# Performance work log

Hardware: AMD Instinct MI355X
Metric: run time of the kernel (lower is better)

The kernel has to match this reference:

```python
import jax, jax.numpy as jnp
import numpy as np

N = 10000
E = 160000
F_IN = 2000
HEADS = 10
C1 = 128      # layer-1 per-head out channels
C2 = 128      # layer-2 per-head out channels (latent_dim)
NEG_SLOPE = 0.2
EPS = 1e-16


def gat_conv(x, W, att_src, att_dst, bias, src, dst, heads, out_ch, concat):
    """PyG-style GATConv (eval mode, self-loops already included in src/dst).
    x: [N, F_in]; W: [F_in, heads*out_ch]; att_*: [heads, out_ch]; bias: [out_dim].
    src/dst: [E'] edge endpoints (message flows src -> dst).
    """
    n = x.shape[0]
    h = (x @ W).reshape(n, heads, out_ch)              # [N, H, C]
    a_src = jnp.einsum('nhc,hc->nh', h, att_src)       # [N, H]
    a_dst = jnp.einsum('nhc,hc->nh', h, att_dst)       # [N, H]
    e = a_src[src] + a_dst[dst]                        # [E', H]
    e = jax.nn.leaky_relu(e, NEG_SLOPE)
    # segment softmax over incoming edges of each destination node
    m = jax.ops.segment_max(e, dst, num_segments=n)    # [N, H]
    ex = jnp.exp(e - m[dst])
    s = jax.ops.segment_sum(ex, dst, num_segments=n)   # [N, H]
    alpha = ex / (s[dst] + EPS)                        # [E', H]
    msg = h[src] * alpha[:, :, None]                   # [E', H, C]
    out = jax.ops.segment_sum(msg, dst, num_segments=n)  # [N, H, C]
    out = out.reshape(n, heads * out_ch) if concat else out.mean(axis=1)
    return out + bias


def setup_inputs() -> dict:
    key = jax.random.key(0)
    ks = jax.random.split(key, 10)
    glorot = lambda k, shape: jax.random.normal(k, shape, jnp.float32) * np.sqrt(2.0 / (shape[0] + shape[-1]))
    x = jax.random.normal(ks[0], (N, F_IN), jnp.float32)
    edge_index = jax.random.randint(ks[1], (2, E), 0, N, jnp.int64)
    W1 = glorot(ks[2], (F_IN, HEADS * C1))
    att_src1 = glorot(ks[3], (HEADS, C1))
    att_dst1 = glorot(ks[4], (HEADS, C1))
    b1 = jnp.zeros((HEADS * C1,), jnp.float32)
    W2 = glorot(ks[5], (HEADS * C1, HEADS * C2))
    att_src2 = glorot(ks[6], (HEADS, C2))
    att_dst2 = glorot(ks[7], (HEADS, C2))
    b2 = jnp.zeros((C2,), jnp.float32)
    return dict(x=x, edge_index=edge_index, W1=W1, att_src1=att_src1,
                att_dst1=att_dst1, b1=b1, W2=W2, att_src2=att_src2,
                att_dst2=att_dst2, b2=b2)


def reference(x, edge_index, W1, att_src1, att_dst1, b1, W2, att_src2, att_dst2, b2):
    n = x.shape[0]
    loops = jnp.arange(n, dtype=edge_index.dtype)
    src = jnp.concatenate([edge_index[0], loops])  # add self-loops (PyG default)
    dst = jnp.concatenate([edge_index[1], loops])
    h = jax.nn.relu(gat_conv(x, W1, att_src1, att_dst1, b1, src, dst, HEADS, C1, True))
    z = jax.nn.relu(gat_conv(h, W2, att_src2, att_dst2, b2, src, dst, HEADS, C2, False))
    return z
```

## Files before the change

kernel.cpp:

```cpp
#include <hip/hip_runtime.h>

typedef unsigned short u16;
typedef __attribute__((ext_vector_type(8))) short bf16x8;
typedef __attribute__((ext_vector_type(4))) float f32x4;
typedef __attribute__((ext_vector_type(4))) unsigned u32x4;

#define NN    10000
#define EE    160000
#define ET    170000
#define FIN   2000
#define MPAD  10112
#define K1PAD 2048
#define NH    1280
#define HEADS 10
#define NT    10
#define NWG   790

__device__ __forceinline__ u16 f32_to_bf16(float f) {
    unsigned u = __float_as_uint(f);
    unsigned r = (u + 0x7fffu + ((u >> 16) & 1u)) >> 16;
    return (u16)r;
}
__device__ __forceinline__ float bf16lo(unsigned pv) { return __uint_as_float(pv << 16); }
__device__ __forceinline__ float bf16hi(unsigned pv) { return __uint_as_float(pv & 0xffff0000u); }

__device__ __forceinline__ void gload16(const u16* g, u16* l) {
    __builtin_amdgcn_global_load_lds(
        (const __attribute__((address_space(1))) void*)g,
        (__attribute__((address_space(3))) void*)l, 16, 0, 0);
}


__global__ __launch_bounds__(256) void k_conv_x(const float* __restrict__ x,
                                                uint2* __restrict__ A1) {
    const int total = MPAD * (K1PAD / 4);
    for (int idx = blockIdx.x * 256 + threadIdx.x; idx < total; idx += gridDim.x * 256) {
        int r = idx >> 9;
        int c = (idx & 511) << 2;
        float4 v = make_float4(0.f, 0.f, 0.f, 0.f);
        if (r < NN && c < FIN) v = *(const float4*)(x + (size_t)r * FIN + c);
        uint2 p;
        p.x = (unsigned)f32_to_bf16(v.x) | ((unsigned)f32_to_bf16(v.y) << 16);
        p.y = (unsigned)f32_to_bf16(v.z) | ((unsigned)f32_to_bf16(v.w) << 16);
        A1[idx] = p;
    }
}

__global__ __launch_bounds__(256) void k_convT(const float* __restrict__ W,
                                               u16* __restrict__ Bt,
                                               int K, int Nn, int Kpad) {
    __shared__ float tile[32][33];
    int k0 = blockIdx.x * 32, n0 = blockIdx.y * 32;
    int tx = threadIdx.x, ty = threadIdx.y;
    #pragma unroll
    for (int i = 0; i < 32; i += 8) {
        int k = k0 + ty + i;
        tile[ty + i][tx] = (k < K) ? W[(size_t)k * Nn + n0 + tx] : 0.f;
    }
    __syncthreads();
    #pragma unroll
    for (int i = 0; i < 32; i += 8) {
        int n = n0 + ty + i, k = k0 + tx;
        Bt[(size_t)n * Kpad + k] = f32_to_bf16(tile[tx][ty + i]);
    }
}


template <bool AHM>
__global__ __launch_bounds__(512) void k_gemm(const u16* __restrict__ A,
                                              const u16* __restrict__ Bt,
                                              u16* __restrict__ Chm,
                                              const int Kpad, const int kTiles) {
    __shared__ __attribute__((aligned(16))) u16 S[32768];
    const int bid = blockIdx.x;
    const int xcd = bid & 7, idx = bid >> 3;
    const int q = NWG >> 3, r = NWG & 7;
    const int L = (xcd < r) ? (xcd * (q + 1) + idx)
                            : (r * (q + 1) + (xcd - r) * q + idx);
    const size_t m0 = (size_t)(L / NT) * 128, n0 = (size_t)(L % NT) * 128;

    const int t = threadIdx.x;
    const int lane = t & 63;
    const int wave = t >> 6;
    const int wr = wave >> 2, wc = wave & 3;

    f32x4 acc[4][2] = {};

    const int srow = t >> 3;
    const int klocal = (((t & 7) ^ ((t >> 3) & 7)) << 3);
    const u16* aRow = AHM ? (A + (m0 + srow) * 128 + klocal)
                          : (A + (m0 + srow) * (size_t)Kpad + klocal);
    const u16* bRow = Bt + (n0 + srow) * (size_t)Kpad + klocal;
    const size_t aStep = AHM ? (size_t)64 * 128 : (size_t)64 * Kpad;
    const size_t bStep = (size_t)64 * Kpad;

#define STAGE(kt_, bufb_) do {                                                   \
        char* db = (char*)S + (bufb_) + wave * 1024;                             \
        const u16* aP;                                                           \
        if (AHM) aP = aRow + (size_t)((kt_) >> 1) * (MPAD << 7) + ((kt_) & 1) * 64; \
        else     aP = aRow + (size_t)(kt_) * 64;                                 \
        const u16* bP = bRow + (size_t)(kt_) * 64;                               \
        gload16(aP,         (u16*)(db));                                         \
        gload16(aP + aStep, (u16*)(db + 8192));                                  \
        gload16(bP,         (u16*)(db + 16384));                                 \
        gload16(bP + bStep, (u16*)(db + 24576));                                 \
    } while (0)

    STAGE(0, 0);

    const int rl = lane & 15;
    const int kchunk = lane >> 4;
    const int xorv = (rl & 7) << 4;
    const int aBase0 = (wr * 64 + rl) * 128;
    const int bBase0 = (wc * 32 + rl) * 128;
    const char* Sb = (const char*)S;

    for (int kt = 0; kt < kTiles; ++kt) {
        asm volatile("s_waitcnt vmcnt(0)" ::: "memory");
        __builtin_amdgcn_s_barrier();
        if (kt + 1 < kTiles) STAGE(kt + 1, ((kt + 1) & 1) * 32768);
        const int bufo = (kt & 1) * 32768;
        #pragma unroll
        for (int ks = 0; ks < 2; ++ks) {
            const int px = (ks * 64 + kchunk * 16) ^ xorv;
            bf16x8 af[4], bfr[2];
            #pragma unroll
            for (int mf = 0; mf < 4; ++mf)
                af[mf] = *(const bf16x8*)(Sb + bufo + aBase0 + mf * 2048 + px);
            #pragma unroll
            for (int nf = 0; nf < 2; ++nf)
                bfr[nf] = *(const bf16x8*)(Sb + bufo + 16384 + bBase0 + nf * 2048 + px);
            #pragma unroll
            for (int mf = 0; mf < 4; ++mf)
                #pragma unroll
                for (int nf = 0; nf < 2; ++nf)
                    acc[mf][nf] = __builtin_amdgcn_mfma_f32_16x16x32_bf16(
                        af[mf], bfr[nf], acc[mf][nf], 0, 0, 0);
        }
    }
#undef STAGE

    u16* Cb = Chm + (size_t)(n0 >> 7) * (MPAD << 7);
    #pragma unroll
    for (int mf = 0; mf < 4; ++mf)
        #pragma unroll
        for (int i = 0; i < 4; ++i) {
            size_t row = m0 + wr * 64 + mf * 16 + (lane >> 4) * 4 + i;
            u16* crow = Cb + row * 128 + wc * 32 + rl;
            #pragma unroll
            for (int nf = 0; nf < 2; ++nf)
                crow[nf * 16] = f32_to_bf16(acc[mf][nf][i]);
        }
}

__global__ __launch_bounds__(256) void k_attn(const u16* __restrict__ Hhm,
                                              const float* __restrict__ att_s,
                                              const float* __restrict__ att_d,
                                              float* __restrict__ a_src,
                                              float* __restrict__ a_dst) {
    const int lane = threadIdx.x & 63;
    const int n = blockIdx.x * 4 + (threadIdx.x >> 6);
    if (n >= NN) return;
    const unsigned* Hd = (const unsigned*)Hhm;
    #pragma unroll
    for (int h = 0; h < HEADS; ++h) {
        unsigned pv = Hd[((size_t)h * MPAD + n) * 64 + lane];
        float v0 = bf16lo(pv), v1 = bf16hi(pv);
        int c = h * 128 + lane * 2;
        float s = v0 * att_s[c] + v1 * att_s[c + 1];
        float d = v0 * att_d[c] + v1 * att_d[c + 1];
        #pragma unroll
        for (int o = 32; o; o >>= 1) { s += __shfl_xor(s, o); d += __shfl_xor(d, o); }
        if (lane == 0) { a_src[n * HEADS + h] = s; a_dst[n * HEADS + h] = d; }
    }
}

__global__ void k_count(const int* __restrict__ ei, int* __restrict__ deg) {
    int e = blockIdx.x * blockDim.x + threadIdx.x;
    if (e >= ET) return;
    int d = (e < EE) ? ei[EE + e] : (e - EE);
    atomicAdd(&deg[d], 1);
}

__global__ __launch_bounds__(256) void k_scan(const int* __restrict__ deg,
                                              int* __restrict__ off,
                                              int* __restrict__ cursor) {
    __shared__ int wt[4];
    const int t = threadIdx.x, lane = t & 63, w = t >> 6;
    const int lo = t * 40;
    const int hi = (lo + 40 < NN) ? lo + 40 : NN;
    int s = 0;
    for (int i = lo; i < hi; ++i) s += deg[i];
    int x = s;
    #pragma unroll
    for (int o = 1; o < 64; o <<= 1) { int y = __shfl_up(x, o); if (lane >= o) x += y; }
    if (lane == 63) wt[w] = x;
    __syncthreads();
    int wp = 0;
    for (int k = 0; k < w; ++k) wp += wt[k];
    int run = wp + x - s;
    for (int i = lo; i < hi; ++i) { off[i] = run; cursor[i] = run; run += deg[i]; }
    if (t == 255) off[NN] = wp + x;
}

__global__ void k_scatter(const int* __restrict__ ei, int* __restrict__ cursor,
                          int* __restrict__ csr_src, int* __restrict__ csr_dst) {
    int e = blockIdx.x * blockDim.x + threadIdx.x;
    if (e >= ET) return;
    int s = (e < EE) ? ei[e] : (e - EE);
    int d = (e < EE) ? ei[EE + e] : (e - EE);
    int pos = atomicAdd(&cursor[d], 1);
    csr_src[pos] = s;
    csr_dst[pos] = d;
}

__global__ __launch_bounds__(256) void k_edgew(const float* __restrict__ a_src,
                                               const float* __restrict__ a_dst,
                                               const int* __restrict__ csr_s,
                                               const int* __restrict__ csr_d,
                                               float* __restrict__ wbuf) {
    int i = blockIdx.x * 256 + threadIdx.x;
    if (i >= ET) return;
    const int s = csr_s[i], d = csr_d[i];
    const float* ps = a_src + (size_t)s * HEADS;
    const float* pd = a_dst + (size_t)d * HEADS;
    #pragma unroll
    for (int h = 0; h < HEADS; ++h) {
        float e = ps[h] + pd[h];
        e = (e >= 0.f) ? e : 0.2f * e;
        wbuf[(size_t)h * ET + i] = __expf(e);
    }
}

template <int LAYER>
__global__ __launch_bounds__(256) void k_agg(const u16* __restrict__ Hhm,
                                             const float* __restrict__ wbuf,
                                             const int* __restrict__ off,
                                             const int* __restrict__ csr,
                                             const float* __restrict__ bias,
                                             unsigned* __restrict__ outp) {
    const int bid = blockIdx.x;
    const int xcd = bid & 7, slot = bid >> 3;
    const int wv = threadIdx.x >> 6, lane = threadIdx.x & 63;
    const int u = slot * 4 + wv;
    if (u >= 3125) return;
    int h, qd;
    if (u < 2500) { h = xcd; qd = u; }
    else {
        int qg = xcd * 625 + (u - 2500);
        h = 8 + (qg >= 2500);
        qd = (qg >= 2500) ? qg - 2500 : qg;
    }
    const int g = lane >> 4, l = lane & 15;
    const int n = qd * 4 + g;
    const int beg = off[n], end = off[n + 1];
    const u16* Hh = Hhm + (size_t)h * (MPAD * 128);
    const float* wp = wbuf + (size_t)h * ET;

    float acc[8] = {};
    float den = 0.f;
    int i = beg;
    for (; i + 1 < end; i += 2) {
        const int s0 = csr[i], s1 = csr[i + 1];
        const float w0 = wp[i], w1 = wp[i + 1];
        const u32x4 v0 = *(const u32x4*)(Hh + (size_t)s0 * 128 + l * 8);
        const u32x4 v1 = *(const u32x4*)(Hh + (size_t)s1 * 128 + l * 8);
        den += w0 + w1;
        #pragma unroll
        for (int j = 0; j < 4; ++j) {
            acc[2 * j]     = fmaf(bf16lo(v0[j]), w0, acc[2 * j]);
            acc[2 * j + 1] = fmaf(bf16hi(v0[j]), w0, acc[2 * j + 1]);
            acc[2 * j]     = fmaf(bf16lo(v1[j]), w1, acc[2 * j]);
            acc[2 * j + 1] = fmaf(bf16hi(v1[j]), w1, acc[2 * j + 1]);
        }
    }
    if (i < end) {
        const int s0 = csr[i];
        const float w0 = wp[i];
        const u32x4 v0 = *(const u32x4*)(Hh + (size_t)s0 * 128 + l * 8);
        den += w0;
        #pragma unroll
        for (int j = 0; j < 4; ++j) {
            acc[2 * j]     = fmaf(bf16lo(v0[j]), w0, acc[2 * j]);
            acc[2 * j + 1] = fmaf(bf16hi(v0[j]), w0, acc[2 * j + 1]);
        }
    }
    const float si = 1.f / (den + 1e-16f);

    u32x4 pk;
    if (LAYER == 1) {
        const int c = h * 128 + l * 8;
        #pragma unroll
        for (int j = 0; j < 4; ++j) {
            float v0 = fmaxf(fmaf(acc[2 * j],     si, bias[c + 2 * j]),     0.f);
            float v1 = fmaxf(fmaf(acc[2 * j + 1], si, bias[c + 2 * j + 1]), 0.f);
            pk[j] = (unsigned)f32_to_bf16(v0) | ((unsigned)f32_to_bf16(v1) << 16);
        }
    } else {
        #pragma unroll
        for (int j = 0; j < 4; ++j) {
            pk[j] = (unsigned)f32_to_bf16(acc[2 * j] * si)
                  | ((unsigned)f32_to_bf16(acc[2 * j + 1] * si) << 16);
        }
    }
    *(u32x4*)(outp + (size_t)h * (MPAD * 64) + (size_t)n * 64 + l * 4) = pk;
}

__global__ __launch_bounds__(256) void k_zpad(unsigned* __restrict__ A2) {
    int idx = blockIdx.x * 256 + threadIdx.x;
    if (idx >= 10 * 112 * 64) return;
    int h = idx / 7168, r = idx - h * 7168;
    int row = NN + (r >> 6), dw = r & 63;
    A2[((size_t)h * MPAD + row) * 64 + dw] = 0u;
}

__global__ __launch_bounds__(256) void k_final(const unsigned* __restrict__ Z,
                                               const float* __restrict__ b2,
                                               float* __restrict__ out) {
    int t = blockIdx.x * 256 + threadIdx.x;
    if (t >= NN * 64) return;
    int n = t >> 6, d = t & 63;
    float s0 = 0.f, s1 = 0.f;
    #pragma unroll
    for (int h = 0; h < HEADS; ++h) {
        unsigned pv = Z[(size_t)h * (MPAD * 64) + (size_t)n * 64 + d];
        s0 += bf16lo(pv);
        s1 += bf16hi(pv);
    }
    float2 z;
    z.x = fmaxf(fmaf(s0, 0.1f, b2[2 * d]),     0.f);
    z.y = fmaxf(fmaf(s1, 0.1f, b2[2 * d + 1]), 0.f);
    *(float2*)(out + (size_t)n * 128 + 2 * d) = z;
}

extern "C" void kernel_launch(void* const* d_in, const int* in_sizes, int n_in,
                              void* d_out, int out_size, void* d_ws, size_t ws_size,
                              hipStream_t stream) {
    const float* x   = (const float*)d_in[0];
    const int*   ei  = (const int*)  d_in[1];
    const float* W1  = (const float*)d_in[2];
    const float* as1 = (const float*)d_in[3];
    const float* ad1 = (const float*)d_in[4];
    const float* b1  = (const float*)d_in[5];
    const float* W2  = (const float*)d_in[6];
    const float* as2 = (const float*)d_in[7];
    const float* ad2 = (const float*)d_in[8];
    const float* b2  = (const float*)d_in[9];

    char* ws = (char*)d_ws;
    const size_t A1_OFF  = 0;
    const size_t A2_OFF  = 0;
    const size_t B2T_OFF = (size_t)MPAD * NH * 2;
    const size_t WB_OFF  = B2T_OFF + (size_t)NH * NH * 2;
    const size_t H_OFF   = (size_t)MPAD * K1PAD * 2;
    const size_t B1T_OFF = H_OFF + (size_t)MPAD * NH * 2;
    size_t o = B1T_OFF + (size_t)NH * K1PAD * 2;
    const size_t AS_OFF  = o; o += 400128;
    const size_t AD_OFF  = o; o += 400128;
    const size_t DEG_OFF = o; o += 40064;
    const size_t OFF_OFF = o; o += 40064;
    const size_t CUR_OFF = o; o += 40064;
    const size_t CSR_OFF = o; o += 680064;
    const size_t CSD_OFF = o; o += 680064;
    if (ws_size < o) return;

    u16*      A1   = (u16*)(ws + A1_OFF);
    unsigned* A2   = (unsigned*)(ws + A2_OFF);
    u16*      B2t  = (u16*)(ws + B2T_OFF);
    float*    wbuf = (float*)(ws + WB_OFF);
    u16*      H    = (u16*)(ws + H_OFF);
    u16*      B1t  = (u16*)(ws + B1T_OFF);
    float*    aS   = (float*)(ws + AS_OFF);
    float*    aD   = (float*)(ws + AD_OFF);
    int*      deg  = (int*)(ws + DEG_OFF);
    int*      offp = (int*)(ws + OFF_OFF);
    int*      cur  = (int*)(ws + CUR_OFF);
    int*      csr  = (int*)(ws + CSR_OFF);
    int*      csd  = (int*)(ws + CSD_OFF);

    hipMemsetAsync(deg, 0, NN * sizeof(int), stream);
    k_count<<<(ET + 255) / 256, 256, 0, stream>>>(ei, deg);
    k_scan<<<1, 256, 0, stream>>>(deg, offp, cur);
    k_scatter<<<(ET + 255) / 256, 256, 0, stream>>>(ei, cur, csr, csd);

    k_conv_x<<<2048, 256, 0, stream>>>(x, (uint2*)A1);
    k_convT<<<dim3(K1PAD / 32, NH / 32), dim3(32, 8), 0, stream>>>(W1, B1t, FIN, NH, K1PAD);
    k_gemm<false><<<NWG, 512, 0, stream>>>(A1, B1t, H, K1PAD, K1PAD / 64);
    k_attn<<<2500, 256, 0, stream>>>(H, as1, ad1, aS, aD);
    k_edgew<<<(ET + 255) / 256, 256, 0, stream>>>(aS, aD, csr, csd, wbuf);
    k_agg<1><<<6256, 256, 0, stream>>>(H, wbuf, offp, csr, b1, A2);
    k_zpad<<<280, 256, 0, stream>>>(A2);

    k_convT<<<dim3(NH / 32, NH / 32), dim3(32, 8), 0, stream>>>(W2, B2t, NH, NH, NH);
    k_gemm<true><<<NWG, 512, 0, stream>>>((u16*)A2, B2t, H, NH, NH / 64);
    k_attn<<<2500, 256, 0, stream>>>(H, as2, ad2, aS, aD);
    k_edgew<<<(ET + 255) / 256, 256, 0, stream>>>(aS, aD, csr, csd, wbuf);
    k_agg<2><<<6256, 256, 0, stream>>>(H, wbuf, offp, csr, b2, A2);
    k_final<<<(NN * 64 + 255) / 256, 256, 0, stream>>>(A2, b2, (float*)d_out);
}
```

Measured before the change: 303.5 us.

## Fuse attention logits into GEMM epilogue and edge weights into aggregation

Attention dot products are now computed in the GEMM epilogue from fp32 accumulators through shuffles and LDS atomics, which removes the separate k_attn pass over H. Edge weights are computed on the fly inside k_agg, which drops the k_edgew kernel, the wbuf array and the csr_dst array. The x/W1 conversion kernels are merged into one launch, and padding zeroing is folded into k_agg<1>. In exchange, the GEMM epilogue does more work, the exp is recomputed per (edge, lane), and a_src is gathered per edge inside the aggregation.

```diff
diff --git a/kernel.cpp b/kernel.cpp
--- a/kernel.cpp
+++ b/kernel.cpp
@@ -30,38 +30,58 @@
         (__attribute__((address_space(3))) void*)l, 16, 0, 0);
 }
 
-
-__global__ __launch_bounds__(256) void k_conv_x(const float* __restrict__ x,
-                                                uint2* __restrict__ A1) {
-    const int total = MPAD * (K1PAD / 4);
-    for (int idx = blockIdx.x * 256 + threadIdx.x; idx < total; idx += gridDim.x * 256) {
-        int r = idx >> 9;
-        int c = (idx & 511) << 2;
-        float4 v = make_float4(0.f, 0.f, 0.f, 0.f);
-        if (r < NN && c < FIN) v = *(const float4*)(x + (size_t)r * FIN + c);
-        uint2 p;
-        p.x = (unsigned)f32_to_bf16(v.x) | ((unsigned)f32_to_bf16(v.y) << 16);
-        p.y = (unsigned)f32_to_bf16(v.z) | ((unsigned)f32_to_bf16(v.w) << 16);
-        A1[idx] = p;
-    }
-}
-
-__global__ __launch_bounds__(256) void k_convT(const float* __restrict__ W,
-                                               u16* __restrict__ Bt,
-                                               int K, int Nn, int Kpad) {
+__global__ __launch_bounds__(256) void k_prep(const float* __restrict__ x,
+                                              uint2* __restrict__ A1,
+                                              const float* __restrict__ W1,
+                                              u16* __restrict__ B1t) {
     __shared__ float tile[32][33];
-    int k0 = blockIdx.x * 32, n0 = blockIdx.y * 32;
-    int tx = threadIdx.x, ty = threadIdx.y;
+    const int bid = blockIdx.x;
+    const int t = threadIdx.x;
+    if (bid < 2048) {
+        const int total = MPAD * (K1PAD / 4);
+        for (int idx = bid * 256 + t; idx < total; idx += 2048 * 256) {
+            int r = idx >> 9;
+            int c = (idx & 511) << 2;
+            float4 v = make_float4(0.f, 0.f, 0.f, 0.f);
+            if (r < NN && c < FIN) v = *(const float4*)(x + (size_t)r * FIN + c);
+            uint2 p;
+            p.x = (unsigned)f32_to_bf16(v.x) | ((unsigned)f32_to_bf16(v.y) << 16);
+            p.y = (unsigned)f32_to_bf16(v.z) | ((unsigned)f32_to_bf16(v.w) << 16);
+            A1[idx] = p;
+        }
+        return;
+    }
+    const int tx = t & 31, ty = t >> 5;
+    int b = bid - 2048;
+    int k0 = (b & 63) * 32, n0 = (b >> 6) * 32;
     #pragma unroll
     for (int i = 0; i < 32; i += 8) {
         int k = k0 + ty + i;
-        tile[ty + i][tx] = (k < K) ? W[(size_t)k * Nn + n0 + tx] : 0.f;
+        tile[ty + i][tx] = (k < FIN) ? W1[(size_t)k * NH + n0 + tx] : 0.f;
     }
     __syncthreads();
     #pragma unroll
     for (int i = 0; i < 32; i += 8) {
         int n = n0 + ty + i, k = k0 + tx;
-        Bt[(size_t)n * Kpad + k] = f32_to_bf16(tile[tx][ty + i]);
+        B1t[(size_t)n * K1PAD + k] = f32_to_bf16(tile[tx][ty + i]);
+    }
+}
+
+__global__ __launch_bounds__(256) void k_prepW2(const float* __restrict__ W2,
+                                                u16* __restrict__ B2t) {
+    __shared__ float tile[32][33];
+    const int t = threadIdx.x;
+    const int tx = t & 31, ty = t >> 5;
+    int b = blockIdx.x;
+    int k0 = (b % 40) * 32, n0 = (b / 40) * 32;
+    #pragma unroll
+    for (int i = 0; i < 32; i += 8)
+        tile[ty + i][tx] = W2[(size_t)(k0 + ty + i) * NH + n0 + tx];
+    __syncthreads();
+    #pragma unroll
+    for (int i = 0; i < 32; i += 8) {
+        int n = n0 + ty + i, k = k0 + tx;
+        B2t[(size_t)n * NH + k] = f32_to_bf16(tile[tx][ty + i]);
     }
 }
 
@@ -70,7 +90,11 @@
 __global__ __launch_bounds__(512) void k_gemm(const u16* __restrict__ A,
                                               const u16* __restrict__ Bt,
                                               u16* __restrict__ Chm,
-                                              const int Kpad, const int kTiles) {
+                                              const int Kpad, const int kTiles,
+                                              const float* __restrict__ att_s,
+                                              const float* __restrict__ att_d,
+                                              float* __restrict__ a_srcp,
+                                              float* __restrict__ a_dstp) {
     __shared__ __attribute__((aligned(16))) u16 S[32768];
     const int bid = blockIdx.x;
     const int xcd = bid & 7, idx = bid >> 3;
@@ -78,6 +102,7 @@
     const int L = (xcd < r) ? (xcd * (q + 1) + idx)
                             : (r * (q + 1) + (xcd - r) * q + idx);
     const size_t m0 = (size_t)(L / NT) * 128, n0 = (size_t)(L % NT) * 128;
+    const int h = (int)(n0 >> 7);
 
     const int t = threadIdx.x;
     const int lane = t & 63;
@@ -140,7 +165,13 @@
     }
 #undef STAGE
 
-    u16* Cb = Chm + (size_t)(n0 >> 7) * (MPAD << 7);
+    float* red_s = (float*)S;
+    float* red_d = red_s + 128;
+    __syncthreads();
+    if (t < 128) { red_s[t] = 0.f; red_d[t] = 0.f; }
+    __syncthreads();
+
+    u16* Cb = Chm + (size_t)h * (MPAD << 7);
     #pragma unroll
     for (int mf = 0; mf < 4; ++mf)
         #pragma unroll
@@ -151,27 +182,35 @@
             for (int nf = 0; nf < 2; ++nf)
                 crow[nf * 16] = f32_to_bf16(acc[mf][nf][i]);
         }
-}
-
-__global__ __launch_bounds__(256) void k_attn(const u16* __restrict__ Hhm,
-                                              const float* __restrict__ att_s,
-                                              const float* __restrict__ att_d,
-                                              float* __restrict__ a_src,
-                                              float* __restrict__ a_dst) {
-    const int lane = threadIdx.x & 63;
-    const int n = blockIdx.x * 4 + (threadIdx.x >> 6);
-    if (n >= NN) return;
-    const unsigned* Hd = (const unsigned*)Hhm;
-    #pragma unroll
-    for (int h = 0; h < HEADS; ++h) {
-        unsigned pv = Hd[((size_t)h * MPAD + n) * 64 + lane];
-        float v0 = bf16lo(pv), v1 = bf16hi(pv);
-        int c = h * 128 + lane * 2;
-        float s = v0 * att_s[c] + v1 * att_s[c + 1];
-        float d = v0 * att_d[c] + v1 * att_d[c + 1];
-        #pragma unroll
-        for (int o = 32; o; o >>= 1) { s += __shfl_xor(s, o); d += __shfl_xor(d, o); }
-        if (lane == 0) { a_src[n * HEADS + h] = s; a_dst[n * HEADS + h] = d; }
+
+    const float as0 = att_s[h * 128 + wc * 32 + rl];
+    const float as1 = att_s[h * 128 + wc * 32 + 16 + rl];
+    const float ad0 = att_d[h * 128 + wc * 32 + rl];
+    const float ad1 = att_d[h * 128 + wc * 32 + 16 + rl];
+    #pragma unroll
+    for (int mf = 0; mf < 4; ++mf)
+        #pragma unroll
+        for (int i = 0; i < 4; ++i) {
+            float ps = acc[mf][0][i] * as0 + acc[mf][1][i] * as1;
+            float pd = acc[mf][0][i] * ad0 + acc[mf][1][i] * ad1;
+            #pragma unroll
+            for (int o = 1; o < 16; o <<= 1) {
+                ps += __shfl_xor(ps, o);
+                pd += __shfl_xor(pd, o);
+            }
+            if (rl == 0) {
+                int rloc = wr * 64 + mf * 16 + (lane >> 4) * 4 + i;
+                atomicAdd(&red_s[rloc], ps);
+                atomicAdd(&red_d[rloc], pd);
+            }
+        }
+    __syncthreads();
+    if (t < 128) {
+        size_t nrow = m0 + t;
+        if (nrow < NN) {
+            a_srcp[nrow * HEADS + h] = red_s[t];
+            a_dstp[nrow * HEADS + h] = red_d[t];
+        }
     }
 }
 
@@ -204,42 +243,31 @@
 }
 
 __global__ void k_scatter(const int* __restrict__ ei, int* __restrict__ cursor,
-                          int* __restrict__ csr_src, int* __restrict__ csr_dst) {
+                          int* __restrict__ csr_src) {
     int e = blockIdx.x * blockDim.x + threadIdx.x;
     if (e >= ET) return;
     int s = (e < EE) ? ei[e] : (e - EE);
     int d = (e < EE) ? ei[EE + e] : (e - EE);
     int pos = atomicAdd(&cursor[d], 1);
     csr_src[pos] = s;
-    csr_dst[pos] = d;
-}
-
-__global__ __launch_bounds__(256) void k_edgew(const float* __restrict__ a_src,
-                                               const float* __restrict__ a_dst,
-                                               const int* __restrict__ csr_s,
-                                               const int* __restrict__ csr_d,
-                                               float* __restrict__ wbuf) {
-    int i = blockIdx.x * 256 + threadIdx.x;
-    if (i >= ET) return;
-    const int s = csr_s[i], d = csr_d[i];
-    const float* ps = a_src + (size_t)s * HEADS;
-    const float* pd = a_dst + (size_t)d * HEADS;
-    #pragma unroll
-    for (int h = 0; h < HEADS; ++h) {
-        float e = ps[h] + pd[h];
-        e = (e >= 0.f) ? e : 0.2f * e;
-        wbuf[(size_t)h * ET + i] = __expf(e);
-    }
 }
 
 template <int LAYER>
 __global__ __launch_bounds__(256) void k_agg(const u16* __restrict__ Hhm,
-                                             const float* __restrict__ wbuf,
+                                             const float* __restrict__ a_src,
+                                             const float* __restrict__ a_dst,
                                              const int* __restrict__ off,
                                              const int* __restrict__ csr,
                                              const float* __restrict__ bias,
                                              unsigned* __restrict__ outp) {
     const int bid = blockIdx.x;
+    if (LAYER == 1 && bid >= 6256) {
+        int idx = (bid - 6256) * 256 + threadIdx.x;
+        int hh = idx / 7168, rr = idx - hh * 7168;
+        int row = NN + (rr >> 6), dw = rr & 63;
+        outp[((size_t)hh * MPAD + row) * 64 + dw] = 0u;
+        return;
+    }
     const int xcd = bid & 7, slot = bid >> 3;
     const int wv = threadIdx.x >> 6, lane = threadIdx.x & 63;
     const int u = slot * 4 + wv;
@@ -255,14 +283,16 @@
     const int n = qd * 4 + g;
     const int beg = off[n], end = off[n + 1];
     const u16* Hh = Hhm + (size_t)h * (MPAD * 128);
-    const float* wp = wbuf + (size_t)h * ET;
+    const float ad = a_dst[n * HEADS + h];
 
     float acc[8] = {};
     float den = 0.f;
     int i = beg;
     for (; i + 1 < end; i += 2) {
         const int s0 = csr[i], s1 = csr[i + 1];
-        const float w0 = wp[i], w1 = wp[i + 1];
+        float e0 = a_src[s0 * HEADS + h] + ad; e0 = (e0 >= 0.f) ? e0 : 0.2f * e0;
+        float e1 = a_src[s1 * HEADS + h] + ad; e1 = (e1 >= 0.f) ? e1 : 0.2f * e1;
+        const float w0 = __expf(e0), w1 = __expf(e1);
         const u32x4 v0 = *(const u32x4*)(Hh + (size_t)s0 * 128 + l * 8);
         const u32x4 v1 = *(const u32x4*)(Hh + (size_t)s1 * 128 + l * 8);
         den += w0 + w1;
@@ -276,7 +306,8 @@
     }
     if (i < end) {
         const int s0 = csr[i];
-        const float w0 = wp[i];
+        float e0 = a_src[s0 * HEADS + h] + ad; e0 = (e0 >= 0.f) ? e0 : 0.2f * e0;
+        const float w0 = __expf(e0);
         const u32x4 v0 = *(const u32x4*)(Hh + (size_t)s0 * 128 + l * 8);
         den += w0;
         #pragma unroll
@@ -304,14 +335,6 @@
         }
     }
     *(u32x4*)(outp + (size_t)h * (MPAD * 64) + (size_t)n * 64 + l * 4) = pk;
-}
-
-__global__ __launch_bounds__(256) void k_zpad(unsigned* __restrict__ A2) {
-    int idx = blockIdx.x * 256 + threadIdx.x;
-    if (idx >= 10 * 112 * 64) return;
-    int h = idx / 7168, r = idx - h * 7168;
-    int row = NN + (r >> 6), dw = r & 63;
-    A2[((size_t)h * MPAD + row) * 64 + dw] = 0u;
 }
 
 __global__ __launch_bounds__(256) void k_final(const unsigned* __restrict__ Z,
@@ -351,7 +374,6 @@
     const size_t A1_OFF  = 0;
     const size_t A2_OFF  = 0;
     const size_t B2T_OFF = (size_t)MPAD * NH * 2;
-    const size_t WB_OFF  = B2T_OFF + (size_t)NH * NH * 2;
     const size_t H_OFF   = (size_t)MPAD * K1PAD * 2;
     const size_t B1T_OFF = H_OFF + (size_t)MPAD * NH * 2;
     size_t o = B1T_OFF + (size_t)NH * K1PAD * 2;
@@ -361,13 +383,11 @@
     const size_t OFF_OFF = o; o += 40064;
     const size_t CUR_OFF = o; o += 40064;
     const size_t CSR_OFF = o; o += 680064;
-    const size_t CSD_OFF = o; o += 680064;
     if (ws_size < o) return;
 
     u16*      A1   = (u16*)(ws + A1_OFF);
     unsigned* A2   = (unsigned*)(ws + A2_OFF);
     u16*      B2t  = (u16*)(ws + B2T_OFF);
-    float*    wbuf = (float*)(ws + WB_OFF);
     u16*      H    = (u16*)(ws + H_OFF);
     u16*      B1t  = (u16*)(ws + B1T_OFF);
     float*    aS   = (float*)(ws + AS_OFF);
@@ -376,25 +396,21 @@
     int*      offp = (int*)(ws + OFF_OFF);
     int*      cur  = (int*)(ws + CUR_OFF);
     int*      csr  = (int*)(ws + CSR_OFF);
-    int*      csd  = (int*)(ws + CSD_OFF);
 
     hipMemsetAsync(deg, 0, NN * sizeof(int), stream);
     k_count<<<(ET + 255) / 256, 256, 0, stream>>>(ei, deg);
     k_scan<<<1, 256, 0, stream>>>(deg, offp, cur);
-    k_scatter<<<(ET + 255) / 256, 256, 0, stream>>>(ei, cur, csr, csd);
-
-    k_conv_x<<<2048, 256, 0, stream>>>(x, (uint2*)A1);
-    k_convT<<<dim3(K1PAD / 32, NH / 32), dim3(32, 8), 0, stream>>>(W1, B1t, FIN, NH, K1PAD);
-    k_gemm<false><<<NWG, 512, 0, stream>>>(A1, B1t, H, K1PAD, K1PAD / 64);
-    k_attn<<<2500, 256, 0, stream>>>(H, as1, ad1, aS, aD);
-    k_edgew<<<(ET + 255) / 256, 256, 0, stream>>>(aS, aD, csr, csd, wbuf);
-    k_agg<1><<<6256, 256, 0, stream>>>(H, wbuf, offp, csr, b1, A2);
-    k_zpad<<<280, 256, 0, stream>>>(A2);
-
-    k_convT<<<dim3(NH / 32, NH / 32), dim3(32, 8), 0, stream>>>(W2, B2t, NH, NH, NH);
-    k_gemm<true><<<NWG, 512, 0, stream>>>((u16*)A2, B2t, H, NH, NH / 64);
-    k_attn<<<2500, 256, 0, stream>>>(H, as2, ad2, aS, aD);
-    k_edgew<<<(ET + 255) / 256, 256, 0, stream>>>(aS, aD, csr, csd, wbuf);
-    k_agg<2><<<6256, 256, 0, stream>>>(H, wbuf, offp, csr, b2, A2);
+    k_scatter<<<(ET + 255) / 256, 256, 0, stream>>>(ei, cur, csr);
+
+    k_prep<<<4608, 256, 0, stream>>>(x, (uint2*)A1, W1, B1t);
+
+    k_gemm<false><<<NWG, 512, 0, stream>>>(A1, B1t, H, K1PAD, K1PAD / 64,
+                                           as1, ad1, aS, aD);
+    k_prepW2<<<1600, 256, 0, stream>>>(W2, B2t);
+    k_agg<1><<<6536, 256, 0, stream>>>(H, aS, aD, offp, csr, b1, A2);
+
+    k_gemm<true><<<NWG, 512, 0, stream>>>((u16*)A2, B2t, H, NH, NH / 64,
+                                          as2, ad2, aS, aD);
+    k_agg<2><<<6256, 256, 0, stream>>>(H, aS, aD, offp, csr, b2, A2);
     k_final<<<(NN * 64 + 255) / 256, 256, 0, stream>>>(A2, b2, (float*)d_out);
 }
```

Measured after the change: 289.4 us. 4.6% less time.
